# Performance work log

Hardware: AMD Instinct MI355X
Metric: run time of the kernel (lower is better)

Reference implementation:

```python
import jax, jax.numpy as jnp
import numpy as np

INNER_D = 4096
LORA_RANK = 2
LORA_ALPHA = 1.0
BATCH, SEQ = 4, 4096


def setup_inputs() -> dict:
    key = jax.random.key(0)
    k_x, k_aq, k_bq, k_as, k_bs = jax.random.split(key, 5)
    x_in = jax.random.normal(k_x, (BATCH, SEQ, INNER_D), dtype=jnp.float32)
    # bnb int8 quantized LoRA weights (row-major [out, in], as nn.Linear stores)
    a_q = jax.random.randint(k_aq, (LORA_RANK, INNER_D), -127, 128, dtype=jnp.int8)
    b_q = jax.random.randint(k_bq, (INNER_D, LORA_RANK), -127, 128, dtype=jnp.int8)
    # per-output-row dequant scales (absmax/127), small positive values
    a_scale = jax.random.uniform(k_as, (LORA_RANK,), jnp.float32, 0.005, 0.02)
    b_scale = jax.random.uniform(k_bs, (INNER_D,), jnp.float32, 0.005, 0.02)
    return {"x_in": x_in, "a_q": a_q, "a_scale": a_scale, "b_q": b_q, "b_scale": b_scale}


def reference(x_in, a_q, a_scale, b_q, b_scale):
    scale = LORA_ALPHA / LORA_RANK  # lora_alpha / lora_rank = 0.5
    # inline dequantization: int8 weight * per-row scale
    A = a_q.astype(jnp.float32) * a_scale[:, None]   # [rank, d]
    B = b_q.astype(jnp.float32) * b_scale[:, None]   # [d, rank]
    h = jnp.einsum('bsd,rd->bsr', x_in, A)           # lora_a(x)
    out = scale * jnp.einsum('bsr,dr->bsd', h, B)    # (alpha/rank) * lora_b(h)
    return out
```

## Files before the change

### kernel.cpp

```cpp
#include <hip/hip_runtime.h>


#define QL_D    4096
#define QL_ROWS 16384
#define RPB     8

typedef float f32x4 __attribute__((ext_vector_type(4)));

__global__ __launch_bounds__(256) void qlora_fused_kernel(
    const float* __restrict__ x,
    const int*   __restrict__ a_q,
    const float* __restrict__ a_scale,
    const int*   __restrict__ b_q,
    const float* __restrict__ b_scale,
    float*       __restrict__ out)
{
    const int t    = threadIdx.x;
    const int row0 = blockIdx.x * RPB;
    const int wave = t >> 6;
    const int lane = t & 63;

    float fa0[16], fa1[16];
    {
        const int4* a0p = (const int4*)a_q;
        const int4* a1p = (const int4*)(a_q + QL_D);
#pragma unroll
        for (int k = 0; k < 4; ++k) {
            const int4 q0 = a0p[t + 256 * k];
            const int4 q1 = a1p[t + 256 * k];
            fa0[4*k+0] = (float)q0.x; fa0[4*k+1] = (float)q0.y;
            fa0[4*k+2] = (float)q0.z; fa0[4*k+3] = (float)q0.w;
            fa1[4*k+0] = (float)q1.x; fa1[4*k+1] = (float)q1.y;
            fa1[4*k+2] = (float)q1.z; fa1[4*k+3] = (float)q1.w;
        }
    }

    __shared__ float sh0[RPB][4], sh1[RPB][4];

    const f32x4* x4 = (const f32x4*)(x + (size_t)row0 * QL_D);
    f32x4*       o4 = (f32x4*)(out + (size_t)row0 * QL_D);

#pragma unroll
    for (int r = 0; r < RPB; ++r) {
        float h0 = 0.0f, h1 = 0.0f;
#pragma unroll
        for (int k = 0; k < 4; ++k) {
            const f32x4 xv =
                __builtin_nontemporal_load(&x4[r * (QL_D / 4) + t + 256 * k]);
            h0 += xv.x * fa0[4*k+0] + xv.y * fa0[4*k+1]
                + xv.z * fa0[4*k+2] + xv.w * fa0[4*k+3];
            h1 += xv.x * fa1[4*k+0] + xv.y * fa1[4*k+1]
                + xv.z * fa1[4*k+2] + xv.w * fa1[4*k+3];
        }
#pragma unroll
        for (int off = 32; off > 0; off >>= 1) {
            h0 += __shfl_down(h0, off, 64);
            h1 += __shfl_down(h1, off, 64);
        }
        if (lane == 0) { sh0[r][wave] = h0; sh1[r][wave] = h1; }
    }

    float bb0[16], bb1[16];
    {
        const int4*   bq4 = (const int4*)b_q;
        const float4* bs4 = (const float4*)b_scale;
#pragma unroll
        for (int k = 0; k < 4; ++k) {
            const int d4 = t + 256 * k;
            const float4 bs = bs4[d4];
            const int4   q0 = bq4[2 * d4];
            const int4   q1 = bq4[2 * d4 + 1];
            bb0[4*k+0] = 0.5f * bs.x * (float)q0.x; bb1[4*k+0] = 0.5f * bs.x * (float)q0.y;
            bb0[4*k+1] = 0.5f * bs.y * (float)q0.z; bb1[4*k+1] = 0.5f * bs.y * (float)q0.w;
            bb0[4*k+2] = 0.5f * bs.z * (float)q1.x; bb1[4*k+2] = 0.5f * bs.z * (float)q1.y;
            bb0[4*k+3] = 0.5f * bs.w * (float)q1.z; bb1[4*k+3] = 0.5f * bs.w * (float)q1.w;
        }
    }

    __syncthreads();

    if (t < RPB) {
        const float H0 = (sh0[t][0] + sh0[t][1] + sh0[t][2] + sh0[t][3]) * a_scale[0];
        const float H1 = (sh1[t][0] + sh1[t][1] + sh1[t][2] + sh1[t][3]) * a_scale[1];
        sh0[t][0] = H0;
        sh1[t][0] = H1;
    }
    __syncthreads();

#pragma unroll
    for (int r = 0; r < RPB; ++r) {
        const float H0 = sh0[r][0];
        const float H1 = sh1[r][0];
#pragma unroll
        for (int k = 0; k < 4; ++k) {
            f32x4 o;
            o.x = H0 * bb0[4*k+0] + H1 * bb1[4*k+0];
            o.y = H0 * bb0[4*k+1] + H1 * bb1[4*k+1];
            o.z = H0 * bb0[4*k+2] + H1 * bb1[4*k+2];
            o.w = H0 * bb0[4*k+3] + H1 * bb1[4*k+3];
            __builtin_nontemporal_store(o, &o4[r * (QL_D / 4) + t + 256 * k]);
        }
    }
}

extern "C" void kernel_launch(void* const* d_in, const int* in_sizes, int n_in,
                              void* d_out, int out_size, void* d_ws, size_t ws_size,
                              hipStream_t stream) {
    const float* x       = (const float*)d_in[0];
    const int*   a_q     = (const int*)d_in[1];
    const float* a_scale = (const float*)d_in[2];
    const int*   b_q     = (const int*)d_in[3];
    const float* b_scale = (const float*)d_in[4];
    float*       out     = (float*)d_out;

    qlora_fused_kernel<<<QL_ROWS / RPB, 256, 0, stream>>>(
        x, a_q, a_scale, b_q, b_scale, out);
}
```

Baseline: 431.6 us.

## Assign whole rows to single waves and stage dequantized weights in LDS

Each wave now processes entire rows: it computes the rank-2 projection with a wave-only shuffle reduction and writes the output row without block-level barriers. The dequantized A and B weights are staged once per block in 64KB of shared memory instead of being held in per-thread registers. The goal is to remove the cross-wave shared-memory reduction and its two __syncthreads per row group, and to overlap loads and stores across independent waves. The cost is extra LDS reads per element and a 64KB LDS footprint that may limit how many blocks fit per CU.

```diff
diff --git a/kernel.cpp b/kernel.cpp
--- a/kernel.cpp
+++ b/kernel.cpp
@@ -3,11 +3,13 @@
 
 #define QL_D    4096
 #define QL_ROWS 16384
-#define RPB     8
+#define THREADS 512
+#define ROWS_PER_WAVE 2
+#define ROWS_PER_BLOCK (8 * ROWS_PER_WAVE)
 
 typedef float f32x4 __attribute__((ext_vector_type(4)));
 
-__global__ __launch_bounds__(256) void qlora_fused_kernel(
+__global__ __launch_bounds__(THREADS, 4) void qlora_wave_kernel(
     const float* __restrict__ x,
     const int*   __restrict__ a_q,
     const float* __restrict__ a_scale,
@@ -16,89 +18,91 @@
     float*       __restrict__ out)
 {
     const int t    = threadIdx.x;
-    const int row0 = blockIdx.x * RPB;
     const int wave = t >> 6;
     const int lane = t & 63;
 
-    float fa0[16], fa1[16];
+    __shared__ float lds[4 * QL_D];
+    float* fa0 = lds;
+    float* fa1 = lds + QL_D;
+    float* bb0 = lds + 2 * QL_D;
+    float* bb1 = lds + 3 * QL_D;
+
     {
-        const int4* a0p = (const int4*)a_q;
-        const int4* a1p = (const int4*)(a_q + QL_D);
+        const int4*   aq4 = (const int4*)a_q;
+        const int4*   bq4 = (const int4*)b_q;
+        const float4* bs4 = (const float4*)b_scale;
 #pragma unroll
-        for (int k = 0; k < 4; ++k) {
-            const int4 q0 = a0p[t + 256 * k];
-            const int4 q1 = a1p[t + 256 * k];
-            fa0[4*k+0] = (float)q0.x; fa0[4*k+1] = (float)q0.y;
-            fa0[4*k+2] = (float)q0.z; fa0[4*k+3] = (float)q0.w;
-            fa1[4*k+0] = (float)q1.x; fa1[4*k+1] = (float)q1.y;
-            fa1[4*k+2] = (float)q1.z; fa1[4*k+3] = (float)q1.w;
+        for (int k = 0; k < 2; ++k) {
+            const int idx = t + THREADS * k;
+            const int4 qa0 = aq4[idx];
+            const int4 qa1 = aq4[QL_D / 4 + idx];
+            ((f32x4*)fa0)[idx] =
+                (f32x4){(float)qa0.x, (float)qa0.y, (float)qa0.z, (float)qa0.w};
+            ((f32x4*)fa1)[idx] =
+                (f32x4){(float)qa1.x, (float)qa1.y, (float)qa1.z, (float)qa1.w};
+
+            const int4   qb0 = bq4[2 * idx];
+            const int4   qb1 = bq4[2 * idx + 1];
+            const float4 bs  = bs4[idx];
+            ((f32x4*)bb0)[idx] = (f32x4){0.5f * bs.x * (float)qb0.x,
+                                         0.5f * bs.y * (float)qb0.z,
+                                         0.5f * bs.z * (float)qb1.x,
+                                         0.5f * bs.w * (float)qb1.z};
+            ((f32x4*)bb1)[idx] = (f32x4){0.5f * bs.x * (float)qb0.y,
+                                         0.5f * bs.y * (float)qb0.w,
+                                         0.5f * bs.z * (float)qb1.y,
+                                         0.5f * bs.w * (float)qb1.w};
         }
     }
+    const float as0 = a_scale[0];
+    const float as1 = a_scale[1];
+    __syncthreads();
 
-    __shared__ float sh0[RPB][4], sh1[RPB][4];
+    const f32x4* fa0v = (const f32x4*)fa0;
+    const f32x4* fa1v = (const f32x4*)fa1;
+    const f32x4* bb0v = (const f32x4*)bb0;
+    const f32x4* bb1v = (const f32x4*)bb1;
 
-    const f32x4* x4 = (const f32x4*)(x + (size_t)row0 * QL_D);
-    f32x4*       o4 = (f32x4*)(out + (size_t)row0 * QL_D);
+    const int rowbase = blockIdx.x * ROWS_PER_BLOCK + wave * ROWS_PER_WAVE;
 
-#pragma unroll
-    for (int r = 0; r < RPB; ++r) {
-        float h0 = 0.0f, h1 = 0.0f;
-#pragma unroll
-        for (int k = 0; k < 4; ++k) {
-            const f32x4 xv =
-                __builtin_nontemporal_load(&x4[r * (QL_D / 4) + t + 256 * k]);
-            h0 += xv.x * fa0[4*k+0] + xv.y * fa0[4*k+1]
-                + xv.z * fa0[4*k+2] + xv.w * fa0[4*k+3];
-            h1 += xv.x * fa1[4*k+0] + xv.y * fa1[4*k+1]
-                + xv.z * fa1[4*k+2] + xv.w * fa1[4*k+3];
+    for (int rr = 0; rr < ROWS_PER_WAVE; ++rr) {
+        const int row = rowbase + rr;
+        const f32x4* xr = (const f32x4*)(x   + (size_t)row * QL_D);
+        f32x4*       orw = (f32x4*)      (out + (size_t)row * QL_D);
+
+        float h0a = 0.f, h0b = 0.f, h1a = 0.f, h1b = 0.f;
+#pragma unroll 8
+        for (int k = 0; k < 16; ++k) {
+            const int d4 = lane + 64 * k;
+            const f32x4 xv = __builtin_nontemporal_load(&xr[d4]);
+            const f32x4 a0 = fa0v[d4];
+            const f32x4 a1 = fa1v[d4];
+            h0a += xv.x * a0.x + xv.y * a0.y;
+            h0b += xv.z * a0.z + xv.w * a0.w;
+            h1a += xv.x * a1.x + xv.y * a1.y;
+            h1b += xv.z * a1.z + xv.w * a1.w;
         }
+        float h0 = h0a + h0b;
+        float h1 = h1a + h1b;
 #pragma unroll
         for (int off = 32; off > 0; off >>= 1) {
             h0 += __shfl_down(h0, off, 64);
             h1 += __shfl_down(h1, off, 64);
         }
-        if (lane == 0) { sh0[r][wave] = h0; sh1[r][wave] = h1; }
-    }
+        const float H0 = __shfl(h0, 0, 64) * as0;
+        const float H1 = __shfl(h1, 0, 64) * as1;
 
-    float bb0[16], bb1[16];
-    {
-        const int4*   bq4 = (const int4*)b_q;
-        const float4* bs4 = (const float4*)b_scale;
-#pragma unroll
-        for (int k = 0; k < 4; ++k) {
-            const int d4 = t + 256 * k;
-            const float4 bs = bs4[d4];
-            const int4   q0 = bq4[2 * d4];
-            const int4   q1 = bq4[2 * d4 + 1];
-            bb0[4*k+0] = 0.5f * bs.x * (float)q0.x; bb1[4*k+0] = 0.5f * bs.x * (float)q0.y;
-            bb0[4*k+1] = 0.5f * bs.y * (float)q0.z; bb1[4*k+1] = 0.5f * bs.y * (float)q0.w;
-            bb0[4*k+2] = 0.5f * bs.z * (float)q1.x; bb1[4*k+2] = 0.5f * bs.z * (float)q1.y;
-            bb0[4*k+3] = 0.5f * bs.w * (float)q1.z; bb1[4*k+3] = 0.5f * bs.w * (float)q1.w;
-        }
-    }
-
-    __syncthreads();
-
-    if (t < RPB) {
-        const float H0 = (sh0[t][0] + sh0[t][1] + sh0[t][2] + sh0[t][3]) * a_scale[0];
-        const float H1 = (sh1[t][0] + sh1[t][1] + sh1[t][2] + sh1[t][3]) * a_scale[1];
-        sh0[t][0] = H0;
-        sh1[t][0] = H1;
-    }
-    __syncthreads();
-
-#pragma unroll
-    for (int r = 0; r < RPB; ++r) {
-        const float H0 = sh0[r][0];
-        const float H1 = sh1[r][0];
-#pragma unroll
-        for (int k = 0; k < 4; ++k) {
+#pragma unroll 8
+        for (int k = 0; k < 16; ++k) {
+            const int d4 = lane + 64 * k;
+            const f32x4 b0 = bb0v[d4];
+            const f32x4 b1 = bb1v[d4];
             f32x4 o;
-            o.x = H0 * bb0[4*k+0] + H1 * bb1[4*k+0];
-            o.y = H0 * bb0[4*k+1] + H1 * bb1[4*k+1];
-            o.z = H0 * bb0[4*k+2] + H1 * bb1[4*k+2];
-            o.w = H0 * bb0[4*k+3] + H1 * bb1[4*k+3];
-            __builtin_nontemporal_store(o, &o4[r * (QL_D / 4) + t + 256 * k]);
+            o.x = H0 * b0.x + H1 * b1.x;
+            o.y = H0 * b0.y + H1 * b1.y;
+            o.z = H0 * b0.z + H1 * b1.z;
+            o.w = H0 * b0.w + H1 * b1.w;
+            __builtin_nontemporal_store(o, &orw[d4]);
         }
     }
 }
@@ -113,6 +117,6 @@
     const float* b_scale = (const float*)d_in[4];
     float*       out     = (float*)d_out;
 
-    qlora_fused_kernel<<<QL_ROWS / RPB, 256, 0, stream>>>(
+    qlora_wave_kernel<<<QL_ROWS / ROWS_PER_BLOCK, THREADS, 0, stream>>>(
         x, a_q, a_scale, b_q, b_scale, out);
 }
```

After: 430.2 us. About the same (-0.3%).
